# Performance work log

Measured on AMD Instinct MI355X. Metric: run time of the kernel, lower is better.

## Reference

```python
import jax, jax.numpy as jnp
import numpy as np

EPS = 1e-5

def _sage(x, src, dst, counts, w_msg, w_root, b, n_nodes):
    # mean-aggregate neighbor features (src -> dst), then linear
    msgs = x[src]                                             # [E, D]
    summed = jax.ops.segment_sum(msgs, dst, num_segments=n_nodes)
    mean = summed / counts                                    # [N, D]
    return mean @ w_msg + x @ w_root + b

def _layernorm(x, gamma, beta):
    mu = jnp.mean(x, axis=-1, keepdims=True)
    var = jnp.var(x, axis=-1, keepdims=True)
    return (x - mu) * jax.lax.rsqrt(var + EPS) * gamma + beta

def setup_inputs() -> dict:
    key = jax.random.key(0)
    N, E, D = 100000, 1600000, 128
    ks = jax.random.split(key, 20)
    z = jax.random.normal(ks[0], (N, D), dtype=jnp.float32)
    edge_index = jax.random.randint(ks[1], (2, E), 0, N, dtype=jnp.int32)
    def lin(k, din, dout):
        return jax.random.normal(k, (din, dout), dtype=jnp.float32) / np.sqrt(din)
    params = {
        'w_msg1': lin(ks[2], 128, 256), 'w_root1': lin(ks[3], 128, 256),
        'b1': jnp.zeros((256,), jnp.float32),
        'g1': jax.random.uniform(ks[4], (256,), jnp.float32, 0.9, 1.1),
        'beta1': jax.random.normal(ks[5], (256,), jnp.float32) * 0.05,
        'w_msg2': lin(ks[6], 256, 256), 'w_root2': lin(ks[7], 256, 256),
        'b2': jnp.zeros((256,), jnp.float32),
        'g2': jax.random.uniform(ks[8], (256,), jnp.float32, 0.9, 1.1),
        'beta2': jax.random.normal(ks[9], (256,), jnp.float32) * 0.05,
        'w_msg3': lin(ks[10], 256, 128), 'w_root3': lin(ks[11], 256, 128),
        'b3': jnp.zeros((128,), jnp.float32),
        'g3': jax.random.uniform(ks[12], (128,), jnp.float32, 0.9, 1.1),
        'beta3': jax.random.normal(ks[13], (128,), jnp.float32) * 0.05,
        'w_msg4': lin(ks[14], 128, 9), 'w_root4': lin(ks[15], 128, 9),
        'b4': jnp.zeros((9,), jnp.float32),
    }
    return {'z': z, 'edge_index': edge_index, **params}

def reference(z, edge_index,
              w_msg1, w_root1, b1, g1, beta1,
              w_msg2, w_root2, b2, g2, beta2,
              w_msg3, w_root3, b3, g3, beta3,
              w_msg4, w_root4, b4):
    N = z.shape[0]
    src, dst = edge_index[0], edge_index[1]
    counts = jax.ops.segment_sum(jnp.ones_like(dst, dtype=z.dtype), dst, num_segments=N)
    counts = jnp.maximum(counts, 1.0)[:, None]
    x = jax.nn.relu(_layernorm(_sage(z, src, dst, counts, w_msg1, w_root1, b1, N), g1, beta1))
    x = jax.nn.relu(_layernorm(_sage(x, src, dst, counts, w_msg2, w_root2, b2, N), g2, beta2))
    x = jax.nn.relu(_layernorm(_sage(x, src, dst, counts, w_msg3, w_root3, b3, N), g3, beta3))
    x = _sage(x, src, dst, counts, w_msg4, w_root4, b4, N)
    return x
```

## Files before the change

### kernel.cpp

```cpp
#include <hip/hip_runtime.h>
#include <hip/hip_bf16.h>


#define EPS 1e-5f

typedef unsigned short u16;
typedef short bf16x8_t __attribute__((ext_vector_type(8)));
typedef float f32x4_t __attribute__((ext_vector_type(4)));

__device__ inline unsigned int bfpack(float a, float b) {
    unsigned int ua = __builtin_bit_cast(unsigned int, a);
    unsigned int ub = __builtin_bit_cast(unsigned int, b);
    ua += 0x7fffu + ((ua >> 16) & 1u);
    ub += 0x7fffu + ((ub >> 16) & 1u);
    return (ua >> 16) | (ub & 0xffff0000u);
}

__device__ inline u16 bfr(float a) {
    unsigned int u = __builtin_bit_cast(unsigned int, a);
    u += 0x7fffu + ((u >> 16) & 1u);
    return (u16)(u >> 16);
}

__device__ inline float bf2f(u16 v) {
    unsigned int u = ((unsigned int)v) << 16;
    return __builtin_bit_cast(float, u);
}

__global__ __launch_bounds__(256) void zero_f4(float4* __restrict__ p, int n4) {
    int i = blockIdx.x * 256 + threadIdx.x;
    if (i < n4) p[i] = make_float4(0.f, 0.f, 0.f, 0.f);
}

__global__ __launch_bounds__(256) void cast_bf16(const float* __restrict__ x,
                                                 u16* __restrict__ y, int n4) {
    int i = blockIdx.x * 256 + threadIdx.x;
    if (i >= n4) return;
    float4 v = ((const float4*)x)[i];
    ((uint2*)y)[i] = make_uint2(bfpack(v.x, v.y), bfpack(v.z, v.w));
}

__global__ __launch_bounds__(256) void transpose_cast(const float* __restrict__ W,
                                                      u16* __restrict__ WT, int K, int N) {
    int idx = blockIdx.x * 256 + threadIdx.x;
    if (idx >= K * N) return;
    int k = idx / N, n = idx - k * N;
    WT[(long)n * K + k] = bfr(W[idx]);
}

__global__ __launch_bounds__(256) void count_deg(const int* __restrict__ dst,
                                                 int* __restrict__ deg, int E) {
    int e = blockIdx.x * 256 + threadIdx.x;
    if (e < E) atomicAdd(&deg[dst[e]], 1);
}

__global__ __launch_bounds__(256) void partial_sums(const int* __restrict__ deg,
                                                    int* __restrict__ partials, int N) {
    __shared__ int lds[4];
    int tid = threadIdx.x;
    int base = blockIdx.x * 1024 + tid * 4;
    int s = 0;
    if (base + 3 < N) {
        int4 v = *(const int4*)(deg + base);
        s = v.x + v.y + v.z + v.w;
    } else {
        for (int i = 0; i < 4; ++i)
            if (base + i < N) s += deg[base + i];
    }
#pragma unroll
    for (int m = 32; m >= 1; m >>= 1) s += __shfl_xor(s, m);
    if ((tid & 63) == 0) lds[tid >> 6] = s;
    __syncthreads();
    if (tid == 0) partials[blockIdx.x] = lds[0] + lds[1] + lds[2] + lds[3];
}

__global__ __launch_bounds__(256) void scan_partials(int* __restrict__ partials, int nb) {
    __shared__ int lds[256];
    int tid = threadIdx.x;
    int v = (tid < nb) ? partials[tid] : 0;
    lds[tid] = v;
    __syncthreads();
    for (int off = 1; off < 256; off <<= 1) {
        int t = (tid >= off) ? lds[tid - off] : 0;
        __syncthreads();
        lds[tid] += t;
        __syncthreads();
    }
    if (tid < nb) partials[tid] = lds[tid] - v;
}

__global__ __launch_bounds__(256) void write_rowptr(const int* __restrict__ deg,
                                                    const int* __restrict__ partials,
                                                    int* __restrict__ rowptr,
                                                    int* __restrict__ cursor,
                                                    float* __restrict__ inv, int N, int E) {
    __shared__ int lds[256];
    int tid = threadIdx.x;
    int base = blockIdx.x * 1024 + tid * 4;
    int d[4];
    int s = 0;
#pragma unroll
    for (int i = 0; i < 4; ++i) {
        d[i] = (base + i < N) ? deg[base + i] : 0;
        s += d[i];
    }
    lds[tid] = s;
    __syncthreads();
    for (int off = 1; off < 256; off <<= 1) {
        int t = (tid >= off) ? lds[tid - off] : 0;
        __syncthreads();
        lds[tid] += t;
        __syncthreads();
    }
    int run = partials[blockIdx.x] + lds[tid] - s;
#pragma unroll
    for (int i = 0; i < 4; ++i) {
        int idx = base + i;
        if (idx < N) {
            rowptr[idx] = run;
            cursor[idx] = run;
            inv[idx] = 1.0f / fmaxf((float)d[i], 1.0f);
            run += d[i];
        }
    }
    if (blockIdx.x == 0 && tid == 0) rowptr[N] = E;
}

__global__ __launch_bounds__(256) void fill_csr(const int* __restrict__ src,
                                                const int* __restrict__ dst,
                                                int* __restrict__ cursor,
                                                int* __restrict__ eidx, int E) {
    int e = blockIdx.x * 256 + threadIdx.x;
    if (e >= E) return;
    int p = atomicAdd(&cursor[dst[e]], 1);
    eidx[p] = src[e];
}

__global__ __launch_bounds__(256) void gather_scale256(const u16* __restrict__ x,
                                                       const int* __restrict__ rowptr,
                                                       const int* __restrict__ eidx,
                                                       const float* __restrict__ inv,
                                                       u16* __restrict__ agg, int N) {
    int wave = threadIdx.x >> 6;
    int lane = threadIdx.x & 63;
    int row = blockIdx.x * 4 + wave;
    if (row >= N) return;
    int beg = rowptr[row], end = rowptr[row + 1];
    const ushort4* xv = (const ushort4*)x;
    float a0 = 0.f, a1 = 0.f, a2 = 0.f, a3 = 0.f;
    float c0 = 0.f, c1 = 0.f, c2 = 0.f, c3 = 0.f;
    int j = beg;
    for (; j + 1 < end; j += 2) {
        ushort4 v = xv[(long)eidx[j] * 64 + lane];
        ushort4 w = xv[(long)eidx[j + 1] * 64 + lane];
        a0 += bf2f(v.x); a1 += bf2f(v.y); a2 += bf2f(v.z); a3 += bf2f(v.w);
        c0 += bf2f(w.x); c1 += bf2f(w.y); c2 += bf2f(w.z); c3 += bf2f(w.w);
    }
    if (j < end) {
        ushort4 v = xv[(long)eidx[j] * 64 + lane];
        a0 += bf2f(v.x); a1 += bf2f(v.y); a2 += bf2f(v.z); a3 += bf2f(v.w);
    }
    float s = inv[row];
    a0 = (a0 + c0) * s; a1 = (a1 + c1) * s; a2 = (a2 + c2) * s; a3 = (a3 + c3) * s;
    ((uint2*)agg)[(long)row * 64 + lane] = make_uint2(bfpack(a0, a1), bfpack(a2, a3));
}

__global__ __launch_bounds__(256) void gather_scale128(const u16* __restrict__ x,
                                                       const int* __restrict__ rowptr,
                                                       const int* __restrict__ eidx,
                                                       const float* __restrict__ inv,
                                                       u16* __restrict__ agg, int N) {
    int half = threadIdx.x >> 5;
    int lane = threadIdx.x & 31;
    int row = blockIdx.x * 8 + half;
    if (row >= N) return;
    int beg = rowptr[row], end = rowptr[row + 1];
    const ushort4* xv = (const ushort4*)x;
    float a0 = 0.f, a1 = 0.f, a2 = 0.f, a3 = 0.f;
    float c0 = 0.f, c1 = 0.f, c2 = 0.f, c3 = 0.f;
    int j = beg;
    for (; j + 1 < end; j += 2) {
        ushort4 v = xv[(long)eidx[j] * 32 + lane];
        ushort4 w = xv[(long)eidx[j + 1] * 32 + lane];
        a0 += bf2f(v.x); a1 += bf2f(v.y); a2 += bf2f(v.z); a3 += bf2f(v.w);
        c0 += bf2f(w.x); c1 += bf2f(w.y); c2 += bf2f(w.z); c3 += bf2f(w.w);
    }
    if (j < end) {
        ushort4 v = xv[(long)eidx[j] * 32 + lane];
        a0 += bf2f(v.x); a1 += bf2f(v.y); a2 += bf2f(v.z); a3 += bf2f(v.w);
    }
    float s = inv[row];
    a0 = (a0 + c0) * s; a1 = (a1 + c1) * s; a2 = (a2 + c2) * s; a3 = (a3 + c3) * s;
    ((uint2*)agg)[(long)row * 32 + lane] = make_uint2(bfpack(a0, a1), bfpack(a2, a3));
}

__global__ __launch_bounds__(256) void gather_add_ln_relu128(const u16* __restrict__ y,
                                                             const int* __restrict__ rowptr,
                                                             const int* __restrict__ eidx,
                                                             const float* __restrict__ inv,
                                                             const u16* __restrict__ r,
                                                             const float* __restrict__ g,
                                                             const float* __restrict__ be,
                                                             u16* __restrict__ out, int N) {
    int half = threadIdx.x >> 5;
    int lane = threadIdx.x & 31;
    int row = blockIdx.x * 8 + half;
    if (row >= N) return;
    int beg = rowptr[row], end = rowptr[row + 1];
    const ushort4* xv = (const ushort4*)y;
    float a0 = 0.f, a1 = 0.f, a2 = 0.f, a3 = 0.f;
    float c0 = 0.f, c1 = 0.f, c2 = 0.f, c3 = 0.f;
    int j = beg;
    for (; j + 1 < end; j += 2) {
        ushort4 v = xv[(long)eidx[j] * 32 + lane];
        ushort4 w = xv[(long)eidx[j + 1] * 32 + lane];
        a0 += bf2f(v.x); a1 += bf2f(v.y); a2 += bf2f(v.z); a3 += bf2f(v.w);
        c0 += bf2f(w.x); c1 += bf2f(w.y); c2 += bf2f(w.z); c3 += bf2f(w.w);
    }
    if (j < end) {
        ushort4 v = xv[(long)eidx[j] * 32 + lane];
        a0 += bf2f(v.x); a1 += bf2f(v.y); a2 += bf2f(v.z); a3 += bf2f(v.w);
    }
    float iv = inv[row];
    ushort4 rr = ((const ushort4*)r)[(long)row * 32 + lane];
    float v0 = (a0 + c0) * iv + bf2f(rr.x);
    float v1 = (a1 + c1) * iv + bf2f(rr.y);
    float v2 = (a2 + c2) * iv + bf2f(rr.z);
    float v3 = (a3 + c3) * iv + bf2f(rr.w);
    float s = v0 + v1 + v2 + v3;
    float ss = v0 * v0 + v1 * v1 + v2 * v2 + v3 * v3;
#pragma unroll
    for (int m = 16; m >= 1; m >>= 1) {
        s += __shfl_xor(s, m);
        ss += __shfl_xor(ss, m);
    }
    float mean = s / 128.f;
    float var = ss / 128.f - mean * mean;
    float rs = rsqrtf(var + EPS);
    int col = lane * 4;
    v0 = fmaxf((v0 - mean) * rs * g[col + 0] + be[col + 0], 0.f);
    v1 = fmaxf((v1 - mean) * rs * g[col + 1] + be[col + 1], 0.f);
    v2 = fmaxf((v2 - mean) * rs * g[col + 2] + be[col + 2], 0.f);
    v3 = fmaxf((v3 - mean) * rs * g[col + 3] + be[col + 3], 0.f);
    ((uint2*)out)[(long)row * 32 + lane] = make_uint2(bfpack(v0, v1), bfpack(v2, v3));
}

__global__ __launch_bounds__(256) void gather9_final(const float* __restrict__ y,
                                                     const int* __restrict__ rowptr,
                                                     const int* __restrict__ eidx,
                                                     const float* __restrict__ inv,
                                                     const float* __restrict__ r,
                                                     float* __restrict__ out, int N) {
    int idx = blockIdx.x * 256 + threadIdx.x;
    int row = idx >> 4;
    int c = idx & 15;
    if (row >= N || c >= 9) return;
    int beg = rowptr[row], end = rowptr[row + 1];
    float a = 0.f;
    for (int j = beg; j < end; ++j) a += y[(long)eidx[j] * 9 + c];
    out[(long)row * 9 + c] = a * inv[row] + r[(long)row * 9 + c];
}

__global__ __launch_bounds__(256) void mfma_gemm_bf(const u16* __restrict__ A1,
                                                    const u16* __restrict__ A2,
                                                    const u16* __restrict__ WT1,
                                                    const u16* __restrict__ WT2,
                                                    const float* __restrict__ bias,
                                                    u16* __restrict__ out, int M, int K,
                                                    int Dout, int two_pass) {
    __shared__ u16 As[128 * 40];
    __shared__ u16 Ws[128 * 40];
    const int tid = threadIdx.x;
    const int bm = blockIdx.x * 128;
    const int bn = blockIdx.y * 128;
    const int l = tid & 63;
    const int w = tid >> 6;
    const int wr = (w & 1) * 64;
    const int wc = (w >> 1) * 64;
    const int ln15 = l & 15;
    const int quad = l >> 4;

    f32x4_t acc[4][4];
#pragma unroll
    for (int i = 0; i < 4; ++i)
#pragma unroll
        for (int j = 0; j < 4; ++j) acc[i][j] = (f32x4_t){0.f, 0.f, 0.f, 0.f};

    const int sr = tid >> 1;
    const int kh = (tid & 1) * 16;

    const int npass = two_pass ? 2 : 1;
    for (int pass = 0; pass < npass; ++pass) {
        const u16* A = pass ? A2 : A1;
        const u16* WT = pass ? WT2 : WT1;
        for (int k0 = 0; k0 < K; k0 += 32) {
            uint4 q0 = make_uint4(0, 0, 0, 0), q1 = make_uint4(0, 0, 0, 0);
            int gr = bm + sr;
            if (gr < M) {
                const u16* ap = A + (long)gr * K + k0 + kh;
                q0 = ((const uint4*)ap)[0];
                q1 = ((const uint4*)ap)[1];
            }
            *(uint4*)(As + sr * 40 + kh) = q0;
            *(uint4*)(As + sr * 40 + kh + 8) = q1;
            const u16* wp = WT + (long)(bn + sr) * K + k0 + kh;
            *(uint4*)(Ws + sr * 40 + kh) = ((const uint4*)wp)[0];
            *(uint4*)(Ws + sr * 40 + kh + 8) = ((const uint4*)wp)[1];
            __syncthreads();

            bf16x8_t a[4], b[4];
#pragma unroll
            for (int i = 0; i < 4; ++i)
                a[i] = *(const bf16x8_t*)(As + (wr + i * 16 + ln15) * 40 + quad * 8);
#pragma unroll
            for (int j = 0; j < 4; ++j)
                b[j] = *(const bf16x8_t*)(Ws + (wc + j * 16 + ln15) * 40 + quad * 8);
#pragma unroll
            for (int i = 0; i < 4; ++i)
#pragma unroll
                for (int j = 0; j < 4; ++j)
                    acc[i][j] = __builtin_amdgcn_mfma_f32_16x16x32_bf16(a[i], b[j], acc[i][j], 0, 0, 0);
            __syncthreads();
        }
    }

#pragma unroll
    for (int j = 0; j < 4; ++j) {
        int col = bn + wc + j * 16 + ln15;
        float bv = bias ? bias[col] : 0.f;
#pragma unroll
        for (int i = 0; i < 4; ++i) {
            int row0 = bm + wr + i * 16 + quad * 4;
            f32x4_t c = acc[i][j];
#pragma unroll
            for (int p = 0; p < 4; ++p) {
                int row = row0 + p;
                if (row < M) out[(long)row * Dout + col] = bfr(c[p] + bv);
            }
        }
    }
}

__global__ __launch_bounds__(256) void mfma_gemm_dual(const u16* __restrict__ A,
                                                      const u16* __restrict__ WTa,
                                                      const u16* __restrict__ WTb,
                                                      const float* __restrict__ biasb,
                                                      u16* __restrict__ outa,
                                                      u16* __restrict__ outb, int M, int K) {
    __shared__ u16 As[128 * 40];
    __shared__ u16 Ws[128 * 40];
    const u16* WT = blockIdx.y ? WTb : WTa;
    u16* out = blockIdx.y ? outb : outa;
    const float* bias = blockIdx.y ? biasb : nullptr;
    const int tid = threadIdx.x;
    const int bm = blockIdx.x * 128;
    const int l = tid & 63;
    const int w = tid >> 6;
    const int wr = (w & 1) * 64;
    const int wc = (w >> 1) * 64;
    const int ln15 = l & 15;
    const int quad = l >> 4;

    f32x4_t acc[4][4];
#pragma unroll
    for (int i = 0; i < 4; ++i)
#pragma unroll
        for (int j = 0; j < 4; ++j) acc[i][j] = (f32x4_t){0.f, 0.f, 0.f, 0.f};

    const int sr = tid >> 1;
    const int kh = (tid & 1) * 16;

    for (int k0 = 0; k0 < K; k0 += 32) {
        uint4 q0 = make_uint4(0, 0, 0, 0), q1 = make_uint4(0, 0, 0, 0);
        int gr = bm + sr;
        if (gr < M) {
            const u16* ap = A + (long)gr * K + k0 + kh;
            q0 = ((const uint4*)ap)[0];
            q1 = ((const uint4*)ap)[1];
        }
        *(uint4*)(As + sr * 40 + kh) = q0;
        *(uint4*)(As + sr * 40 + kh + 8) = q1;
        const u16* wp = WT + (long)sr * K + k0 + kh;
        *(uint4*)(Ws + sr * 40 + kh) = ((const uint4*)wp)[0];
        *(uint4*)(Ws + sr * 40 + kh + 8) = ((const uint4*)wp)[1];
        __syncthreads();

        bf16x8_t a[4], b[4];
#pragma unroll
        for (int i = 0; i < 4; ++i)
            a[i] = *(const bf16x8_t*)(As + (wr + i * 16 + ln15) * 40 + quad * 8);
#pragma unroll
        for (int j = 0; j < 4; ++j)
            b[j] = *(const bf16x8_t*)(Ws + (wc + j * 16 + ln15) * 40 + quad * 8);
#pragma unroll
        for (int i = 0; i < 4; ++i)
#pragma unroll
            for (int j = 0; j < 4; ++j)
                acc[i][j] = __builtin_amdgcn_mfma_f32_16x16x32_bf16(a[i], b[j], acc[i][j], 0, 0, 0);
        __syncthreads();
    }

#pragma unroll
    for (int j = 0; j < 4; ++j) {
        int col = wc + j * 16 + ln15;
        float bv = bias ? bias[col] : 0.f;
#pragma unroll
        for (int i = 0; i < 4; ++i) {
            int row0 = bm + wr + i * 16 + quad * 4;
            f32x4_t c = acc[i][j];
#pragma unroll
            for (int p = 0; p < 4; ++p) {
                int row = row0 + p;
                if (row < M) out[(long)row * 128 + col] = bfr(c[p] + bv);
            }
        }
    }
}

__global__ __launch_bounds__(256) void mfma_gemm_wide_bf(const u16* A1,
                                                         const u16* __restrict__ A2,
                                                         const u16* __restrict__ WT1,
                                                         const u16* __restrict__ WT2,
                                                         const float* __restrict__ bias,
                                                         u16* out, int M, int K) {
    __shared__ u16 As[64 * 40];
    __shared__ u16 Ws[256 * 40];
    const int tid = threadIdx.x;
    const int bm = blockIdx.x * 64;
    const int l = tid & 63;
    const int w = tid >> 6;
    const int wr = (w & 1) * 32;
    const int wc = (w >> 1) * 128;
    const int ln15 = l & 15;
    const int quad = l >> 4;

    f32x4_t acc[2][8];
#pragma unroll
    for (int i = 0; i < 2; ++i)
#pragma unroll
        for (int j = 0; j < 8; ++j) acc[i][j] = (f32x4_t){0.f, 0.f, 0.f, 0.f};

    const int ar = tid >> 2;
    const int akh = (tid & 3) * 8;

    for (int pass = 0; pass < 2; ++pass) {
        const u16* A = pass ? A2 : A1;
        const u16* WT = pass ? WT2 : WT1;
        for (int k0 = 0; k0 < K; k0 += 32) {
            uint4 q0 = make_uint4(0, 0, 0, 0);
            int gr = bm + ar;
            if (gr < M) q0 = *(const uint4*)(A + (long)gr * K + k0 + akh);
            *(uint4*)(As + ar * 40 + akh) = q0;
            const u16* wp = WT + (long)tid * K + k0;
            *(uint4*)(Ws + tid * 40 + 0) = ((const uint4*)wp)[0];
            *(uint4*)(Ws + tid * 40 + 8) = ((const uint4*)wp)[1];
            *(uint4*)(Ws + tid * 40 + 16) = ((const uint4*)wp)[2];
            *(uint4*)(Ws + tid * 40 + 24) = ((const uint4*)wp)[3];
            __syncthreads();

            bf16x8_t a[2], b[8];
#pragma unroll
            for (int i = 0; i < 2; ++i)
                a[i] = *(const bf16x8_t*)(As + (wr + i * 16 + ln15) * 40 + quad * 8);
#pragma unroll
            for (int j = 0; j < 8; ++j)
                b[j] = *(const bf16x8_t*)(Ws + (wc + j * 16 + ln15) * 40 + quad * 8);
#pragma unroll
            for (int i = 0; i < 2; ++i)
#pragma unroll
                for (int j = 0; j < 8; ++j)
                    acc[i][j] = __builtin_amdgcn_mfma_f32_16x16x32_bf16(a[i], b[j], acc[i][j], 0, 0, 0);
            __syncthreads();
        }
    }

#pragma unroll
    for (int j = 0; j < 8; ++j) {
        int col = wc + j * 16 + ln15;
        float bv = bias[col];
#pragma unroll
        for (int i = 0; i < 2; ++i) {
            int row0 = bm + wr + i * 16 + quad * 4;
            f32x4_t c = acc[i][j];
#pragma unroll
            for (int p = 0; p < 4; ++p) {
                int row = row0 + p;
                if (row < M) out[(long)row * 256 + col] = bfr(c[p] + bv);
            }
        }
    }
}

__global__ __launch_bounds__(256) void ln_relu_bf256(u16* __restrict__ h,
                                                     const float* __restrict__ g,
                                                     const float* __restrict__ be, int M) {
    int wave = threadIdx.x >> 6;
    int lane = threadIdx.x & 63;
    int row = blockIdx.x * 4 + wave;
    if (row >= M) return;
    u16* p = h + (long)row * 256 + lane * 4;
    ushort4 ld = *(const ushort4*)p;
    float v0 = bf2f(ld.x), v1 = bf2f(ld.y), v2 = bf2f(ld.z), v3 = bf2f(ld.w);
    float s = v0 + v1 + v2 + v3;
    float ss = v0 * v0 + v1 * v1 + v2 * v2 + v3 * v3;
#pragma unroll
    for (int m = 32; m >= 1; m >>= 1) {
        s += __shfl_xor(s, m);
        ss += __shfl_xor(ss, m);
    }
    float mean = s / 256.f;
    float var = ss / 256.f - mean * mean;
    float rs = rsqrtf(var + EPS);
    int col = lane * 4;
    v0 = fmaxf((v0 - mean) * rs * g[col + 0] + be[col + 0], 0.f);
    v1 = fmaxf((v1 - mean) * rs * g[col + 1] + be[col + 1], 0.f);
    v2 = fmaxf((v2 - mean) * rs * g[col + 2] + be[col + 2], 0.f);
    v3 = fmaxf((v3 - mean) * rs * g[col + 3] + be[col + 3], 0.f);
    *(uint2*)p = make_uint2(bfpack(v0, v1), bfpack(v2, v3));
}

__global__ __launch_bounds__(320) void gemm4_bf(const u16* __restrict__ x,
                                                const float* __restrict__ wm,
                                                const float* __restrict__ wrt,
                                                const float* __restrict__ b,
                                                float* __restrict__ y, float* __restrict__ r,
                                                int M) {
    __shared__ float xs[16][132];
    __shared__ float ws[128][20];
    int tid = threadIdx.x;
    int m0 = blockIdx.x * 16;
    for (int idx = tid; idx < 16 * 128; idx += 320) {
        int rr = idx >> 7, kk = idx & 127;
        int gm = m0 + rr;
        xs[rr][kk] = (gm < M) ? bf2f(x[(long)gm * 128 + kk]) : 0.f;
    }
    for (int idx = tid; idx < 128 * 18; idx += 320) {
        int kk = idx / 18, cc = idx % 18;
        ws[kk][cc] = (cc < 9) ? wm[kk * 9 + cc] : wrt[kk * 9 + cc - 9];
    }
    __syncthreads();
    if (tid < 288) {
        int rr = tid / 18, cc = tid % 18;
        float acc = 0.f;
#pragma unroll 8
        for (int kk = 0; kk < 128; ++kk) acc += xs[rr][kk] * ws[kk][cc];
        int gm = m0 + rr;
        if (gm < M) {
            if (cc < 9) y[(long)gm * 9 + cc] = acc;
            else r[(long)gm * 9 + cc - 9] = acc + b[cc - 9];
        }
    }
}

static inline int cdiv(long a, long b) { return (int)((a + b - 1) / b); }

extern "C" void kernel_launch(void* const* d_in, const int* in_sizes, int n_in,
                              void* d_out, int out_size, void* d_ws, size_t ws_size,
                              hipStream_t stream) {
    const int N = in_sizes[0] / 128;
    const int E = in_sizes[1] / 2;

    const float* z = (const float*)d_in[0];
    const int* ei = (const int*)d_in[1];
    const int* src = ei;
    const int* dstp = ei + E;
    const float* wm1 = (const float*)d_in[2];
    const float* wr1 = (const float*)d_in[3];
    const float* b1 = (const float*)d_in[4];
    const float* g1 = (const float*)d_in[5];
    const float* be1 = (const float*)d_in[6];
    const float* wm2 = (const float*)d_in[7];
    const float* wr2 = (const float*)d_in[8];
    const float* b2 = (const float*)d_in[9];
    const float* g2 = (const float*)d_in[10];
    const float* be2 = (const float*)d_in[11];
    const float* wm3 = (const float*)d_in[12];
    const float* wr3 = (const float*)d_in[13];
    const float* b3 = (const float*)d_in[14];
    const float* g3 = (const float*)d_in[15];
    const float* be3 = (const float*)d_in[16];
    const float* wm4 = (const float*)d_in[17];
    const float* wr4 = (const float*)d_in[18];
    const float* b4 = (const float*)d_in[19];
    float* out = (float*)d_out;

    u16* aggh2 = (u16*)d_ws;
    u16* h1b = aggh2 + (size_t)N * 256;
    u16* zb = h1b + (size_t)N * 256;
    u16* agg1 = zb + (size_t)N * 128;
    float* inv = (float*)(agg1 + (size_t)N * 128);
    int* deg = (int*)(inv + N);
    int* rowptr = deg + N + 4;
    int* cursor = rowptr + N + 4;
    int* partials = cursor + N + 4;
    int* eidx = partials + 256;
    u16* wt1m = (u16*)(eidx + E);
    u16* wt1r = wt1m + 256 * 128;
    u16* wt2m = wt1r + 256 * 128;
    u16* wt2r = wt2m + 256 * 256;
    u16* wt3m = wt2r + 256 * 256;
    u16* wt3r = wt3m + 128 * 256;

    u16* y3b = agg1;
    u16* r3b = zb;
    u16* h3b = h1b;
    float* y4 = (float*)aggh2;
    float* r4 = y4 + (size_t)N * 9;

    const int nscan = cdiv(N, 1024);

    cast_bf16<<<cdiv((long)N * 32, 256), 256, 0, stream>>>(z, zb, N * 32);
    zero_f4<<<cdiv(N, 1024), 256, 0, stream>>>((float4*)deg, cdiv(N, 4));
    count_deg<<<cdiv(E, 256), 256, 0, stream>>>(dstp, deg, E);
    partial_sums<<<nscan, 256, 0, stream>>>(deg, partials, N);
    scan_partials<<<1, 256, 0, stream>>>(partials, nscan);
    write_rowptr<<<nscan, 256, 0, stream>>>(deg, partials, rowptr, cursor, inv, N, E);
    fill_csr<<<cdiv(E, 256), 256, 0, stream>>>(src, dstp, cursor, eidx, E);
    transpose_cast<<<cdiv(128 * 256, 256), 256, 0, stream>>>(wm1, wt1m, 128, 256);
    transpose_cast<<<cdiv(128 * 256, 256), 256, 0, stream>>>(wr1, wt1r, 128, 256);
    transpose_cast<<<cdiv(256 * 256, 256), 256, 0, stream>>>(wm2, wt2m, 256, 256);
    transpose_cast<<<cdiv(256 * 256, 256), 256, 0, stream>>>(wr2, wt2r, 256, 256);
    transpose_cast<<<cdiv(256 * 128, 256), 256, 0, stream>>>(wm3, wt3m, 256, 128);
    transpose_cast<<<cdiv(256 * 128, 256), 256, 0, stream>>>(wr3, wt3r, 256, 128);

    gather_scale128<<<cdiv(N, 8), 256, 0, stream>>>(zb, rowptr, eidx, inv, agg1, N);
    {
        dim3 g(cdiv(N, 128), 2);
        mfma_gemm_bf<<<g, 256, 0, stream>>>(agg1, zb, wt1m, wt1r, b1, h1b, N, 128, 256, 1);
    }
    ln_relu_bf256<<<cdiv(N, 4), 256, 0, stream>>>(h1b, g1, be1, N);

    gather_scale256<<<cdiv(N, 4), 256, 0, stream>>>(h1b, rowptr, eidx, inv, aggh2, N);
    mfma_gemm_wide_bf<<<cdiv(N, 64), 256, 0, stream>>>(aggh2, h1b, wt2m, wt2r, b2, aggh2, N, 256);
    ln_relu_bf256<<<cdiv(N, 4), 256, 0, stream>>>(aggh2, g2, be2, N);

    {
        dim3 g(cdiv(N, 128), 2);
        mfma_gemm_dual<<<g, 256, 0, stream>>>(aggh2, wt3m, wt3r, b3, y3b, r3b, N, 256);
    }
    gather_add_ln_relu128<<<cdiv(N, 8), 256, 0, stream>>>(y3b, rowptr, eidx, inv, r3b, g3, be3, h3b, N);

    gemm4_bf<<<cdiv(N, 16), 320, 0, stream>>>(h3b, wm4, wr4, b4, y4, r4, N);
    gather9_final<<<cdiv((long)N * 16, 256), 256, 0, stream>>>(y4, rowptr, eidx, inv, r4, out, N);
}
```

Measured before the change: 929.8 us.

## Fuse LayerNorm+ReLU into wide GEMMs, batch weight transposes, store layer-4 messages as bf16

```diff
diff --git a/kernel.cpp b/kernel.cpp
--- a/kernel.cpp
+++ b/kernel.cpp
@@ -40,12 +40,18 @@
     ((uint2*)y)[i] = make_uint2(bfpack(v.x, v.y), bfpack(v.z, v.w));
 }
 
-__global__ __launch_bounds__(256) void transpose_cast(const float* __restrict__ W,
-                                                      u16* __restrict__ WT, int K, int N) {
+struct WtJobs {
+    const float* W[6];
+    u16* WT[6];
+    int K[6], N[6];
+};
+__global__ __launch_bounds__(256) void transpose_cast6(WtJobs jobs) {
+    int j = blockIdx.y;
     int idx = blockIdx.x * 256 + threadIdx.x;
-    if (idx >= K * N) return;
-    int k = idx / N, n = idx - k * N;
-    WT[(long)n * K + k] = bfr(W[idx]);
+    int K = jobs.K[j], Nn = jobs.N[j];
+    if (idx >= K * Nn) return;
+    int k = idx / Nn, n = idx - k * Nn;
+    jobs.WT[j][(long)n * K + k] = bfr(jobs.W[j][idx]);
 }
 
 __global__ __launch_bounds__(256) void count_deg(const int* __restrict__ dst,
@@ -133,7 +139,7 @@
     int e = blockIdx.x * 256 + threadIdx.x;
     if (e >= E) return;
     int p = atomicAdd(&cursor[dst[e]], 1);
-    eidx[p] = src[e];
+    atomicExch(&eidx[p], src[e]);
 }
 
 __global__ __launch_bounds__(256) void gather_scale256(const u16* __restrict__ x,
@@ -245,7 +251,7 @@
     ((uint2*)out)[(long)row * 32 + lane] = make_uint2(bfpack(v0, v1), bfpack(v2, v3));
 }
 
-__global__ __launch_bounds__(256) void gather9_final(const float* __restrict__ y,
+__global__ __launch_bounds__(256) void gather9_final(const u16* __restrict__ y,
                                                      const int* __restrict__ rowptr,
                                                      const int* __restrict__ eidx,
                                                      const float* __restrict__ inv,
@@ -257,87 +263,107 @@
     if (row >= N || c >= 9) return;
     int beg = rowptr[row], end = rowptr[row + 1];
     float a = 0.f;
-    for (int j = beg; j < end; ++j) a += y[(long)eidx[j] * 9 + c];
+    for (int j = beg; j < end; ++j) a += bf2f(y[(long)eidx[j] * 9 + c]);
     out[(long)row * 9 + c] = a * inv[row] + r[(long)row * 9 + c];
 }
 
-__global__ __launch_bounds__(256) void mfma_gemm_bf(const u16* __restrict__ A1,
-                                                    const u16* __restrict__ A2,
-                                                    const u16* __restrict__ WT1,
-                                                    const u16* __restrict__ WT2,
-                                                    const float* __restrict__ bias,
-                                                    u16* __restrict__ out, int M, int K,
-                                                    int Dout, int two_pass) {
-    __shared__ u16 As[128 * 40];
-    __shared__ u16 Ws[128 * 40];
+__global__ __launch_bounds__(256) void mfma_gemm_wide_ln(const u16* A1,
+                                                         const u16* __restrict__ A2,
+                                                         const u16* __restrict__ WT1,
+                                                         const u16* __restrict__ WT2,
+                                                         const float* __restrict__ bias,
+                                                         const float* __restrict__ g,
+                                                         const float* __restrict__ be,
+                                                         u16* out, int M, int K) {
+    __shared__ __align__(16) u16 smem[64 * 260];
+    u16* As = smem;
+    u16* Ws = smem + 64 * 40;
     const int tid = threadIdx.x;
-    const int bm = blockIdx.x * 128;
-    const int bn = blockIdx.y * 128;
+    const int bm = blockIdx.x * 64;
     const int l = tid & 63;
     const int w = tid >> 6;
-    const int wr = (w & 1) * 64;
-    const int wc = (w >> 1) * 64;
+    const int wr = (w & 1) * 32;
+    const int wc = (w >> 1) * 128;
     const int ln15 = l & 15;
     const int quad = l >> 4;
 
-    f32x4_t acc[4][4];
-#pragma unroll
-    for (int i = 0; i < 4; ++i)
-#pragma unroll
-        for (int j = 0; j < 4; ++j) acc[i][j] = (f32x4_t){0.f, 0.f, 0.f, 0.f};
-
-    const int sr = tid >> 1;
-    const int kh = (tid & 1) * 16;
-
-    const int npass = two_pass ? 2 : 1;
-    for (int pass = 0; pass < npass; ++pass) {
+    f32x4_t acc[2][8];
+#pragma unroll
+    for (int i = 0; i < 2; ++i)
+#pragma unroll
+        for (int j = 0; j < 8; ++j) acc[i][j] = (f32x4_t){0.f, 0.f, 0.f, 0.f};
+
+    const int ar = tid >> 2;
+    const int akh = (tid & 3) * 8;
+
+    for (int pass = 0; pass < 2; ++pass) {
         const u16* A = pass ? A2 : A1;
         const u16* WT = pass ? WT2 : WT1;
         for (int k0 = 0; k0 < K; k0 += 32) {
-            uint4 q0 = make_uint4(0, 0, 0, 0), q1 = make_uint4(0, 0, 0, 0);
-            int gr = bm + sr;
-            if (gr < M) {
-                const u16* ap = A + (long)gr * K + k0 + kh;
-                q0 = ((const uint4*)ap)[0];
-                q1 = ((const uint4*)ap)[1];
-            }
-            *(uint4*)(As + sr * 40 + kh) = q0;
-            *(uint4*)(As + sr * 40 + kh + 8) = q1;
-            const u16* wp = WT + (long)(bn + sr) * K + k0 + kh;
-            *(uint4*)(Ws + sr * 40 + kh) = ((const uint4*)wp)[0];
-            *(uint4*)(Ws + sr * 40 + kh + 8) = ((const uint4*)wp)[1];
+            uint4 q0 = make_uint4(0, 0, 0, 0);
+            int gr = bm + ar;
+            if (gr < M) q0 = *(const uint4*)(A + (long)gr * K + k0 + akh);
+            *(uint4*)(As + ar * 40 + akh) = q0;
+            const u16* wp = WT + (long)tid * K + k0;
+            *(uint4*)(Ws + tid * 40 + 0) = ((const uint4*)wp)[0];
+            *(uint4*)(Ws + tid * 40 + 8) = ((const uint4*)wp)[1];
+            *(uint4*)(Ws + tid * 40 + 16) = ((const uint4*)wp)[2];
+            *(uint4*)(Ws + tid * 40 + 24) = ((const uint4*)wp)[3];
             __syncthreads();
 
-            bf16x8_t a[4], b[4];
-#pragma unroll
-            for (int i = 0; i < 4; ++i)
+            bf16x8_t a[2], b[8];
+#pragma unroll
+            for (int i = 0; i < 2; ++i)
                 a[i] = *(const bf16x8_t*)(As + (wr + i * 16 + ln15) * 40 + quad * 8);
 #pragma unroll
-            for (int j = 0; j < 4; ++j)
+            for (int j = 0; j < 8; ++j)
                 b[j] = *(const bf16x8_t*)(Ws + (wc + j * 16 + ln15) * 40 + quad * 8);
 #pragma unroll
-            for (int i = 0; i < 4; ++i)
-#pragma unroll
-                for (int j = 0; j < 4; ++j)
+            for (int i = 0; i < 2; ++i)
+#pragma unroll
+                for (int j = 0; j < 8; ++j)
                     acc[i][j] = __builtin_amdgcn_mfma_f32_16x16x32_bf16(a[i], b[j], acc[i][j], 0, 0, 0);
             __syncthreads();
         }
     }
 
 #pragma unroll
-    for (int j = 0; j < 4; ++j) {
-        int col = bn + wc + j * 16 + ln15;
-        float bv = bias ? bias[col] : 0.f;
-#pragma unroll
-        for (int i = 0; i < 4; ++i) {
-            int row0 = bm + wr + i * 16 + quad * 4;
+    for (int j = 0; j < 8; ++j) {
+        int col = wc + j * 16 + ln15;
+        float bv = bias[col];
+#pragma unroll
+        for (int i = 0; i < 2; ++i) {
+            int row0 = wr + i * 16 + quad * 4;
             f32x4_t c = acc[i][j];
 #pragma unroll
-            for (int p = 0; p < 4; ++p) {
-                int row = row0 + p;
-                if (row < M) out[(long)row * Dout + col] = bfr(c[p] + bv);
-            }
-        }
+            for (int p = 0; p < 4; ++p) smem[(row0 + p) * 260 + col] = bfr(c[p] + bv);
+        }
+    }
+    __syncthreads();
+
+    float4 g4 = *(const float4*)&g[l * 4];
+    float4 be4 = *(const float4*)&be[l * 4];
+    for (int rr = 0; rr < 16; ++rr) {
+        int lrow = w * 16 + rr;
+        int grow = bm + lrow;
+        if (grow >= M) break;
+        ushort4 ld = *(const ushort4*)(smem + lrow * 260 + l * 4);
+        float v0 = bf2f(ld.x), v1 = bf2f(ld.y), v2 = bf2f(ld.z), v3 = bf2f(ld.w);
+        float s = v0 + v1 + v2 + v3;
+        float ss = v0 * v0 + v1 * v1 + v2 * v2 + v3 * v3;
+#pragma unroll
+        for (int m = 32; m >= 1; m >>= 1) {
+            s += __shfl_xor(s, m);
+            ss += __shfl_xor(ss, m);
+        }
+        float mean = s / 256.f;
+        float var = ss / 256.f - mean * mean;
+        float rs = rsqrtf(var + EPS);
+        v0 = fmaxf((v0 - mean) * rs * g4.x + be4.x, 0.f);
+        v1 = fmaxf((v1 - mean) * rs * g4.y + be4.y, 0.f);
+        v2 = fmaxf((v2 - mean) * rs * g4.z + be4.z, 0.f);
+        v3 = fmaxf((v3 - mean) * rs * g4.w + be4.w, 0.f);
+        ((uint2*)out)[(long)grow * 64 + l] = make_uint2(bfpack(v0, v1), bfpack(v2, v3));
     }
 }
 
@@ -417,113 +443,11 @@
     }
 }
 
-__global__ __launch_bounds__(256) void mfma_gemm_wide_bf(const u16* A1,
-                                                         const u16* __restrict__ A2,
-                                                         const u16* __restrict__ WT1,
-                                                         const u16* __restrict__ WT2,
-                                                         const float* __restrict__ bias,
-                                                         u16* out, int M, int K) {
-    __shared__ u16 As[64 * 40];
-    __shared__ u16 Ws[256 * 40];
-    const int tid = threadIdx.x;
-    const int bm = blockIdx.x * 64;
-    const int l = tid & 63;
-    const int w = tid >> 6;
-    const int wr = (w & 1) * 32;
-    const int wc = (w >> 1) * 128;
-    const int ln15 = l & 15;
-    const int quad = l >> 4;
-
-    f32x4_t acc[2][8];
-#pragma unroll
-    for (int i = 0; i < 2; ++i)
-#pragma unroll
-        for (int j = 0; j < 8; ++j) acc[i][j] = (f32x4_t){0.f, 0.f, 0.f, 0.f};
-
-    const int ar = tid >> 2;
-    const int akh = (tid & 3) * 8;
-
-    for (int pass = 0; pass < 2; ++pass) {
-        const u16* A = pass ? A2 : A1;
-        const u16* WT = pass ? WT2 : WT1;
-        for (int k0 = 0; k0 < K; k0 += 32) {
-            uint4 q0 = make_uint4(0, 0, 0, 0);
-            int gr = bm + ar;
-            if (gr < M) q0 = *(const uint4*)(A + (long)gr * K + k0 + akh);
-            *(uint4*)(As + ar * 40 + akh) = q0;
-            const u16* wp = WT + (long)tid * K + k0;
-            *(uint4*)(Ws + tid * 40 + 0) = ((const uint4*)wp)[0];
-            *(uint4*)(Ws + tid * 40 + 8) = ((const uint4*)wp)[1];
-            *(uint4*)(Ws + tid * 40 + 16) = ((const uint4*)wp)[2];
-            *(uint4*)(Ws + tid * 40 + 24) = ((const uint4*)wp)[3];
-            __syncthreads();
-
-            bf16x8_t a[2], b[8];
-#pragma unroll
-            for (int i = 0; i < 2; ++i)
-                a[i] = *(const bf16x8_t*)(As + (wr + i * 16 + ln15) * 40 + quad * 8);
-#pragma unroll
-            for (int j = 0; j < 8; ++j)
-                b[j] = *(const bf16x8_t*)(Ws + (wc + j * 16 + ln15) * 40 + quad * 8);
-#pragma unroll
-            for (int i = 0; i < 2; ++i)
-#pragma unroll
-                for (int j = 0; j < 8; ++j)
-                    acc[i][j] = __builtin_amdgcn_mfma_f32_16x16x32_bf16(a[i], b[j], acc[i][j], 0, 0, 0);
-            __syncthreads();
-        }
-    }
-
-#pragma unroll
-    for (int j = 0; j < 8; ++j) {
-        int col = wc + j * 16 + ln15;
-        float bv = bias[col];
-#pragma unroll
-        for (int i = 0; i < 2; ++i) {
-            int row0 = bm + wr + i * 16 + quad * 4;
-            f32x4_t c = acc[i][j];
-#pragma unroll
-            for (int p = 0; p < 4; ++p) {
-                int row = row0 + p;
-                if (row < M) out[(long)row * 256 + col] = bfr(c[p] + bv);
-            }
-        }
-    }
-}
-
-__global__ __launch_bounds__(256) void ln_relu_bf256(u16* __restrict__ h,
-                                                     const float* __restrict__ g,
-                                                     const float* __restrict__ be, int M) {
-    int wave = threadIdx.x >> 6;
-    int lane = threadIdx.x & 63;
-    int row = blockIdx.x * 4 + wave;
-    if (row >= M) return;
-    u16* p = h + (long)row * 256 + lane * 4;
-    ushort4 ld = *(const ushort4*)p;
-    float v0 = bf2f(ld.x), v1 = bf2f(ld.y), v2 = bf2f(ld.z), v3 = bf2f(ld.w);
-    float s = v0 + v1 + v2 + v3;
-    float ss = v0 * v0 + v1 * v1 + v2 * v2 + v3 * v3;
-#pragma unroll
-    for (int m = 32; m >= 1; m >>= 1) {
-        s += __shfl_xor(s, m);
-        ss += __shfl_xor(ss, m);
-    }
-    float mean = s / 256.f;
-    float var = ss / 256.f - mean * mean;
-    float rs = rsqrtf(var + EPS);
-    int col = lane * 4;
-    v0 = fmaxf((v0 - mean) * rs * g[col + 0] + be[col + 0], 0.f);
-    v1 = fmaxf((v1 - mean) * rs * g[col + 1] + be[col + 1], 0.f);
-    v2 = fmaxf((v2 - mean) * rs * g[col + 2] + be[col + 2], 0.f);
-    v3 = fmaxf((v3 - mean) * rs * g[col + 3] + be[col + 3], 0.f);
-    *(uint2*)p = make_uint2(bfpack(v0, v1), bfpack(v2, v3));
-}
-
 __global__ __launch_bounds__(320) void gemm4_bf(const u16* __restrict__ x,
                                                 const float* __restrict__ wm,
                                                 const float* __restrict__ wrt,
                                                 const float* __restrict__ b,
-                                                float* __restrict__ y, float* __restrict__ r,
+                                                u16* __restrict__ y, float* __restrict__ r,
                                                 int M) {
     __shared__ float xs[16][132];
     __shared__ float ws[128][20];
@@ -546,7 +470,7 @@
         for (int kk = 0; kk < 128; ++kk) acc += xs[rr][kk] * ws[kk][cc];
         int gm = m0 + rr;
         if (gm < M) {
-            if (cc < 9) y[(long)gm * 9 + cc] = acc;
+            if (cc < 9) y[(long)gm * 9 + cc] = bfr(acc);
             else r[(long)gm * 9 + cc - 9] = acc + b[cc - 9];
         }
     }
@@ -604,8 +528,8 @@
     u16* y3b = agg1;
     u16* r3b = zb;
     u16* h3b = h1b;
-    float* y4 = (float*)aggh2;
-    float* r4 = y4 + (size_t)N * 9;
+    u16* y4 = aggh2;
+    float* r4 = (float*)(aggh2 + (size_t)N * 16);
 
     const int nscan = cdiv(N, 1024);
 
@@ -616,29 +540,32 @@
     scan_partials<<<1, 256, 0, stream>>>(partials, nscan);
     write_rowptr<<<nscan, 256, 0, stream>>>(deg, partials, rowptr, cursor, inv, N, E);
     fill_csr<<<cdiv(E, 256), 256, 0, stream>>>(src, dstp, cursor, eidx, E);
-    transpose_cast<<<cdiv(128 * 256, 256), 256, 0, stream>>>(wm1, wt1m, 128, 256);
-    transpose_cast<<<cdiv(128 * 256, 256), 256, 0, stream>>>(wr1, wt1r, 128, 256);
-    transpose_cast<<<cdiv(256 * 256, 256), 256, 0, stream>>>(wm2, wt2m, 256, 256);
-    transpose_cast<<<cdiv(256 * 256, 256), 256, 0, stream>>>(wr2, wt2r, 256, 256);
-    transpose_cast<<<cdiv(256 * 128, 256), 256, 0, stream>>>(wm3, wt3m, 256, 128);
-    transpose_cast<<<cdiv(256 * 128, 256), 256, 0, stream>>>(wr3, wt3r, 256, 128);
+    {
+        WtJobs jobs;
+        jobs.W[0] = wm1; jobs.WT[0] = wt1m; jobs.K[0] = 128; jobs.N[0] = 256;
+        jobs.W[1] = wr1; jobs.WT[1] = wt1r; jobs.K[1] = 128; jobs.N[1] = 256;
+        jobs.W[2] = wm2; jobs.WT[2] = wt2m; jobs.K[2] = 256; jobs.N[2] = 256;
+        jobs.W[3] = wr2; jobs.WT[3] = wt2r; jobs.K[3] = 256; jobs.N[3] = 256;
+        jobs.W[4] = wm3; jobs.WT[4] = wt3m; jobs.K[4] = 256; jobs.N[4] = 128;
+        jobs.W[5] = wr3; jobs.WT[5] = wt3r; jobs.K[5] = 256; jobs.N[5] = 128;
+        dim3 g(256, 6);
+        transpose_cast6<<<g, 256, 0, stream>>>(jobs);
+    }
 
     gather_scale128<<<cdiv(N, 8), 256, 0, stream>>>(zb, rowptr, eidx, inv, agg1, N);
-    {
-        dim3 g(cdiv(N, 128), 2);
-        mfma_gemm_bf<<<g, 256, 0, stream>>>(agg1, zb, wt1m, wt1r, b1, h1b, N, 128, 256, 1);
-    }
-    ln_relu_bf256<<<cdiv(N, 4), 256, 0, stream>>>(h1b, g1, be1, N);
+    mfma_gemm_wide_ln<<<cdiv(N, 64), 256, 0, stream>>>(agg1, zb, wt1m, wt1r, b1, g1, be1,
+                                                       h1b, N, 128);
 
     gather_scale256<<<cdiv(N, 4), 256, 0, stream>>>(h1b, rowptr, eidx, inv, aggh2, N);
-    mfma_gemm_wide_bf<<<cdiv(N, 64), 256, 0, stream>>>(aggh2, h1b, wt2m, wt2r, b2, aggh2, N, 256);
-    ln_relu_bf256<<<cdiv(N, 4), 256, 0, stream>>>(aggh2, g2, be2, N);
+    mfma_gemm_wide_ln<<<cdiv(N, 64), 256, 0, stream>>>(aggh2, h1b, wt2m, wt2r, b2, g2, be2,
+                                                       aggh2, N, 256);
 
     {
         dim3 g(cdiv(N, 128), 2);
         mfma_gemm_dual<<<g, 256, 0, stream>>>(aggh2, wt3m, wt3r, b3, y3b, r3b, N, 256);
     }
-    gather_add_ln_relu128<<<cdiv(N, 8), 256, 0, stream>>>(y3b, rowptr, eidx, inv, r3b, g3, be3, h3b, N);
+    gather_add_ln_relu128<<<cdiv(N, 8), 256, 0, stream>>>(y3b, rowptr, eidx, inv, r3b, g3,
+                                                          be3, h3b, N);
 
     gemm4_bf<<<cdiv(N, 16), 320, 0, stream>>>(h3b, wm4, wr4, b4, y4, r4, N);
     gather9_final<<<cdiv((long)N * 16, 256), 256, 0, stream>>>(y4, rowptr, eidx, inv, r4, out, N);
```

Result: faster. 891.6 us (-4.1%).
